# Kernel optimization log

Hardware: AMD Instinct MI355X
Metric: run time of the kernel (lower is better)

Reference implementation:

```python
import jax, jax.numpy as jnp
import numpy as np

EPS = 1e-08

def setup_inputs() -> dict:
    key = jax.random.key(0)
    k1, k2, k3 = jax.random.split(key, 3)
    R, N, E, F, O = 4, 10000, 2000, 128, 128
    X = jax.random.normal(k1, (N, F), dtype=jnp.float32)
    H = jax.random.uniform(k2, (R, N, E), dtype=jnp.float32)
    W = jax.random.normal(k3, (R, F, O), dtype=jnp.float32) * (1.0 / np.sqrt(F))
    relation_importance = jnp.ones((R,), dtype=jnp.float32)
    bias = jnp.zeros((O,), dtype=jnp.float32)
    return {"X": X, "H": H, "W": W, "relation_importance": relation_importance, "bias": bias}

def reference(X, H, W, relation_importance, bias):
    # Per-relation degree normalization applied as elementwise row/col scaling
    # (mathematically identical to diag(Dv^-1/2) @ H @ diag(De^-1/2)).
    D_v = jnp.sum(H, axis=2)                      # [R, N] node degrees
    D_e = jnp.sum(H, axis=1)                      # [R, E] hyperedge degrees
    dv_is = jnp.power(D_v + EPS, -0.5)            # [R, N]
    de_is = jnp.power(D_e + EPS, -0.5)            # [R, E]
    theta = H * dv_is[:, :, None] * de_is[:, None, :]   # [R, N, E]
    # theta @ theta.T @ X  computed right-to-left to avoid an NxN intermediate
    tX = jnp.einsum('rne,nf->ref', theta, X)      # [R, E, F]
    H_norm = jnp.einsum('rne,ref->rnf', theta, tX)  # [R, N, F]
    out = jnp.einsum('rnf,rfo->rno', H_norm, W)   # [R, N, O]
    gate = jax.nn.sigmoid(relation_importance)    # [R]
    final = jnp.sum(out * gate[:, None, None], axis=0)  # [N, O]
    return final + bias
```

## Files before the change

### kernel.cpp

```cpp
#include <hip/hip_runtime.h>
#include <hip/hip_bf16.h>

constexpr int R  = 4;
constexpr int NN = 10000;
constexpr int EE = 2000;
constexpr int FF = 128;
constexpr int OO = 128;
#define EPSV 1e-8f

typedef __attribute__((ext_vector_type(8))) short   bf16x8;
typedef __attribute__((ext_vector_type(4))) float   f32x4;

__device__ inline unsigned short f2bf(float x) {
    unsigned int u = __float_as_uint(x);
    unsigned int r = (u + 0x7fffu + ((u >> 16) & 1u)) >> 16;
    return (unsigned short)r;
}

__global__ __launch_bounds__(256) void k_deg(const float* __restrict__ H,
                                             float* __restrict__ dv_is,
                                             float* __restrict__ De) {
    const int r    = blockIdx.y;
    const int row0 = blockIdx.x * 16;
    const int t    = threadIdx.x;
    const float* Hr = H + (size_t)r * NN * EE;

    float cax[4] = {0.f, 0.f, 0.f, 0.f};
    float cay[4] = {0.f, 0.f, 0.f, 0.f};
    float rp[16];

    for (int j = 0; j < 16; ++j) {
        const float2* Hrow2 = (const float2*)(Hr + (size_t)(row0 + j) * EE);
        float s = 0.f;
#pragma unroll
        for (int i = 0; i < 4; ++i) {
            int e2 = t + 256 * i;
            if (e2 < EE / 2) {
                float2 v = Hrow2[e2];
                s += v.x + v.y;
                cax[i] += v.x;
                cay[i] += v.y;
            }
        }
        rp[j] = s;
    }

    __shared__ float lds[16][257];
#pragma unroll
    for (int j = 0; j < 16; ++j) lds[j][t] = rp[j];
    __syncthreads();
    const int jj = t >> 4, s0 = t & 15;
    float x = 0.f;
#pragma unroll
    for (int k = 0; k < 16; ++k) x += lds[jj][s0 + 16 * k];
    __syncthreads();
    lds[jj][s0] = x;
    __syncthreads();
    if (t < 16) {
        float sum = 0.f;
#pragma unroll
        for (int s = 0; s < 16; ++s) sum += lds[t][s];
        dv_is[r * NN + row0 + t] = rsqrtf(sum + EPSV);
    }

#pragma unroll
    for (int i = 0; i < 4; ++i) {
        int e2 = t + 256 * i;
        if (e2 < EE / 2) {
            atomicAdd(&De[r * EE + 2 * e2 + 0], cax[i]);
            atomicAdd(&De[r * EE + 2 * e2 + 1], cay[i]);
        }
    }
}

__global__ __launch_bounds__(256) void k_xt(const float* __restrict__ X,
                                            unsigned short* __restrict__ Xbt) {
    const int n0 = blockIdx.x * 64;
    const int f0 = blockIdx.y * 64;
    __shared__ float tile[64][65];
    const int t = threadIdx.x;
    {
        int nl = t >> 2;
        int fl = (t & 3) * 16;
        int n  = n0 + nl;
#pragma unroll
        for (int c = 0; c < 4; ++c) {
            float4 v = make_float4(0.f, 0.f, 0.f, 0.f);
            if (n < NN) v = *(const float4*)(X + (size_t)n * FF + f0 + fl + 4 * c);
            tile[nl][fl + 4 * c + 0] = v.x;
            tile[nl][fl + 4 * c + 1] = v.y;
            tile[nl][fl + 4 * c + 2] = v.z;
            tile[nl][fl + 4 * c + 3] = v.w;
        }
    }
    __syncthreads();
    {
        int fr = t >> 2;
        int nc = (t & 3) * 16;
        unsigned short u[16];
#pragma unroll
        for (int k = 0; k < 16; ++k) u[k] = f2bf(tile[nc + k][fr]);
        int f = f0 + fr;
        int nb = n0 + nc;
        unsigned short* dst = Xbt + (size_t)f * NN + nb;
        if (nb + 15 < NN) {
            uint4 p0, p1;
            p0.x = (unsigned)u[0]  | ((unsigned)u[1]  << 16);
            p0.y = (unsigned)u[2]  | ((unsigned)u[3]  << 16);
            p0.z = (unsigned)u[4]  | ((unsigned)u[5]  << 16);
            p0.w = (unsigned)u[6]  | ((unsigned)u[7]  << 16);
            p1.x = (unsigned)u[8]  | ((unsigned)u[9]  << 16);
            p1.y = (unsigned)u[10] | ((unsigned)u[11] << 16);
            p1.z = (unsigned)u[12] | ((unsigned)u[13] << 16);
            p1.w = (unsigned)u[14] | ((unsigned)u[15] << 16);
            *(uint4*)(dst)     = p0;
            *(uint4*)(dst + 8) = p1;
        } else {
#pragma unroll
            for (int k = 0; k < 16; ++k)
                if (nb + k < NN) dst[k] = u[k];
        }
    }
}

__device__ inline int lds_addr(int row, int byte_col) {
    return row * 128 + (byte_col ^ ((row & 7) << 4));
}

__global__ __launch_bounds__(256) void k_gemm1(const float* __restrict__ H,
                                               const unsigned short* __restrict__ Xbt,
                                               const float* __restrict__ dv_is,
                                               const float* __restrict__ De,
                                               float* __restrict__ T) {
    const int r  = blockIdx.y;
    const int e0 = blockIdx.x * 32;
    __shared__ unsigned short lA[32 * 64];
    __shared__ unsigned short lB[128 * 64];
    char* lAb = (char*)lA;
    char* lBb = (char*)lB;

    const int t = threadIdx.x;
    const int wave = t >> 6, lane = t & 63;
    const float* Hr  = H + (size_t)r * NN * EE;
    const float* dvr = dv_is + r * NN;

    f32x4 acc[2][2];
#pragma unroll
    for (int m = 0; m < 2; ++m)
#pragma unroll
        for (int n = 0; n < 2; ++n) acc[m][n] = (f32x4){0.f, 0.f, 0.f, 0.f};

    const int eg = (t & 7) * 4;
    const int np = t >> 3;
    const int bf = t >> 1;
    const int bh = (t & 1) * 32;

    for (int k0 = 0; k0 < NN; k0 += 64) {
        __syncthreads();
        {
            int n_ = k0 + 2 * np;
            float va[4] = {0.f, 0.f, 0.f, 0.f};
            float vb[4] = {0.f, 0.f, 0.f, 0.f};
            float d0 = 0.f, d1 = 0.f;
            const int eb = e0 + eg;
            const bool efull = (eb + 3) < EE;
            if (n_ < NN) {
                d0 = dvr[n_];
                const float* p = Hr + (size_t)n_ * EE + eb;
                if (efull) {
                    float4 v = *(const float4*)p;
                    va[0] = v.x; va[1] = v.y; va[2] = v.z; va[3] = v.w;
                } else {
#pragma unroll
                    for (int c = 0; c < 4; ++c)
                        if (eb + c < EE) va[c] = p[c];
                }
            }
            if (n_ + 1 < NN) {
                d1 = dvr[n_ + 1];
                const float* p = Hr + (size_t)(n_ + 1) * EE + eb;
                if (efull) {
                    float4 v = *(const float4*)p;
                    vb[0] = v.x; vb[1] = v.y; vb[2] = v.z; vb[3] = v.w;
                } else {
#pragma unroll
                    for (int c = 0; c < 4; ++c)
                        if (eb + c < EE) vb[c] = p[c];
                }
            }
#pragma unroll
            for (int j = 0; j < 4; ++j) {
                int row = eg + j;
                unsigned pk = (unsigned)f2bf(va[j] * d0) |
                              ((unsigned)f2bf(vb[j] * d1) << 16);
                *(unsigned*)(lAb + lds_addr(row, 4 * np)) = pk;
            }
        }
        {
#pragma unroll
            for (int j2 = 0; j2 < 4; ++j2) {
                int nb = bh + 8 * j2;
                uint4 v = *(const uint4*)(Xbt + (size_t)bf * NN + k0 + nb);
                *(uint4*)(lBb + lds_addr(bf, 2 * nb)) = v;
            }
        }
        __syncthreads();
        {
            const int kb = (lane >> 4) * 16;
#pragma unroll
            for (int kk = 0; kk < 2; ++kk) {
                bf16x8 a[2], b[2];
#pragma unroll
                for (int m = 0; m < 2; ++m) {
                    int row = (lane & 15) + 16 * m;
                    a[m] = *(const bf16x8*)(lAb + lds_addr(row, kk * 64 + kb));
                }
#pragma unroll
                for (int nf = 0; nf < 2; ++nf) {
                    int row = wave * 32 + (lane & 15) + 16 * nf;
                    b[nf] = *(const bf16x8*)(lBb + lds_addr(row, kk * 64 + kb));
                }
#pragma unroll
                for (int m = 0; m < 2; ++m)
#pragma unroll
                    for (int nf = 0; nf < 2; ++nf)
                        acc[m][nf] = __builtin_amdgcn_mfma_f32_16x16x32_bf16(
                            a[m], b[nf], acc[m][nf], 0, 0, 0);
            }
        }
    }
#pragma unroll
    for (int m = 0; m < 2; ++m) {
        int e_b = e0 + 16 * m + (lane >> 4) * 4;
#pragma unroll
        for (int j = 0; j < 4; ++j) {
            int e = e_b + j;
            if (e < EE) {
                float de2 = 1.0f / (De[r * EE + e] + EPSV);
#pragma unroll
                for (int nf = 0; nf < 2; ++nf) {
                    int f = wave * 32 + 16 * nf + (lane & 15);
                    T[((size_t)r * EE + e) * FF + f] = acc[m][nf][j] * de2;
                }
            }
        }
    }
}

__global__ __launch_bounds__(256) void k_v(const float* __restrict__ T,
                                           const float* __restrict__ W,
                                           const float* __restrict__ ri,
                                           unsigned short* __restrict__ Vt) {
    const int r  = blockIdx.y;
    const int e0 = blockIdx.x * 32;
    const float gate = 1.f / (1.f + expf(-ri[r]));
    __shared__ float lT[32][129];
    const int t = threadIdx.x;
    {
        int el = t >> 3, fl = (t & 7) * 16;
        int e = e0 + el;
#pragma unroll
        for (int c = 0; c < 4; ++c) {
            float4 v = make_float4(0.f, 0.f, 0.f, 0.f);
            if (e < EE) v = *(const float4*)(T + ((size_t)r * EE + e) * FF + fl + 4 * c);
            lT[el][fl + 4 * c + 0] = v.x;
            lT[el][fl + 4 * c + 1] = v.y;
            lT[el][fl + 4 * c + 2] = v.z;
            lT[el][fl + 4 * c + 3] = v.w;
        }
    }
    __syncthreads();
    const int o  = t & 127;
    const int eh = t >> 7;
    float acc[16];
#pragma unroll
    for (int k = 0; k < 16; ++k) acc[k] = 0.f;
    const float* Wr = W + (size_t)r * FF * OO + o;
#pragma unroll 4
    for (int f = 0; f < FF; ++f) {
        float w = Wr[(size_t)f * OO];
#pragma unroll
        for (int k = 0; k < 16; ++k) acc[k] += lT[eh * 16 + k][f] * w;
    }
    const int ebase = e0 + eh * 16;
    unsigned short* dst = Vt + ((size_t)r * OO + o) * EE + ebase;
    if (ebase + 15 < EE) {
        unsigned short u[16];
#pragma unroll
        for (int k = 0; k < 16; ++k) u[k] = f2bf(gate * acc[k]);
        uint4 p0, p1;
        p0.x = (unsigned)u[0]  | ((unsigned)u[1]  << 16);
        p0.y = (unsigned)u[2]  | ((unsigned)u[3]  << 16);
        p0.z = (unsigned)u[4]  | ((unsigned)u[5]  << 16);
        p0.w = (unsigned)u[6]  | ((unsigned)u[7]  << 16);
        p1.x = (unsigned)u[8]  | ((unsigned)u[9]  << 16);
        p1.y = (unsigned)u[10] | ((unsigned)u[11] << 16);
        p1.z = (unsigned)u[12] | ((unsigned)u[13] << 16);
        p1.w = (unsigned)u[14] | ((unsigned)u[15] << 16);
        *(uint4*)(dst)     = p0;
        *(uint4*)(dst + 8) = p1;
    } else {
#pragma unroll
        for (int k = 0; k < 16; ++k)
            if (ebase + k < EE) dst[k] = f2bf(gate * acc[k]);
    }
}

__global__ __launch_bounds__(256) void k_gemm2(const float* __restrict__ H,
                                               const unsigned short* __restrict__ Vt,
                                               const float* __restrict__ dv_is,
                                               const float* __restrict__ bias,
                                               float* __restrict__ out) {
    const int n0 = blockIdx.x * 16;
    __shared__ unsigned short lA[16 * 64];
    __shared__ unsigned short lB[128 * 64];
    char* lAb = (char*)lA;
    char* lBb = (char*)lB;

    const int t = threadIdx.x;
    const int wave = t >> 6, lane = t & 63;

    f32x4 acc[2];
    acc[0] = (f32x4){0.f, 0.f, 0.f, 0.f};
    acc[1] = (f32x4){0.f, 0.f, 0.f, 0.f};

    const int nl  = t >> 4;
    const int el4 = (t & 15) * 4;
    const int bo  = t >> 1;
    const int bh  = (t & 1) * 32;

    for (int r = 0; r < R; ++r) {
        const float* Hrow = H + ((size_t)r * NN + n0 + nl) * EE;
        const float dv = dv_is[r * NN + n0 + nl];
        const unsigned short* Vtr = Vt + (size_t)r * OO * EE;

        for (int ek = 0; ek < 2048; ek += 64) {
            __syncthreads();
            {
                int e = ek + el4;
                float va[4] = {0.f, 0.f, 0.f, 0.f};
                if (e + 3 < EE) {
                    float4 v = *(const float4*)(Hrow + e);
                    va[0] = v.x; va[1] = v.y; va[2] = v.z; va[3] = v.w;
                } else {
#pragma unroll
                    for (int c = 0; c < 4; ++c)
                        if (e + c < EE) va[c] = Hrow[e + c];
                }
                uint2 pk;
                pk.x = (unsigned)f2bf(va[0] * dv) | ((unsigned)f2bf(va[1] * dv) << 16);
                pk.y = (unsigned)f2bf(va[2] * dv) | ((unsigned)f2bf(va[3] * dv) << 16);
                *(uint2*)(lAb + lds_addr(nl, 2 * el4)) = pk;
            }
            {
#pragma unroll
                for (int j2 = 0; j2 < 4; ++j2) {
                    int ebo = bh + 8 * j2;
                    uint4 v = *(const uint4*)(Vtr + (size_t)bo * EE + ek + ebo);
                    *(uint4*)(lBb + lds_addr(bo, 2 * ebo)) = v;
                }
            }
            __syncthreads();
            {
                const int kb = (lane >> 4) * 16;
#pragma unroll
                for (int kk = 0; kk < 2; ++kk) {
                    int arow = lane & 15;
                    bf16x8 a = *(const bf16x8*)(lAb + lds_addr(arow, kk * 64 + kb));
#pragma unroll
                    for (int nf = 0; nf < 2; ++nf) {
                        int row = wave * 32 + (lane & 15) + 16 * nf;
                        bf16x8 b = *(const bf16x8*)(lBb + lds_addr(row, kk * 64 + kb));
                        acc[nf] = __builtin_amdgcn_mfma_f32_16x16x32_bf16(
                            a, b, acc[nf], 0, 0, 0);
                    }
                }
            }
        }
    }
    {
        int nrow = n0 + (lane >> 4) * 4;
#pragma unroll
        for (int nf = 0; nf < 2; ++nf) {
            int o = wave * 32 + 16 * nf + (lane & 15);
            float bv = bias[o];
#pragma unroll
            for (int j = 0; j < 4; ++j)
                out[(size_t)(nrow + j) * OO + o] = acc[nf][j] + bv;
        }
    }
}

extern "C" void kernel_launch(void* const* d_in, const int* in_sizes, int n_in,
                              void* d_out, int out_size, void* d_ws, size_t ws_size,
                              hipStream_t stream) {
    const float* X    = (const float*)d_in[0];
    const float* H    = (const float*)d_in[1];
    const float* W    = (const float*)d_in[2];
    const float* ri   = (const float*)d_in[3];
    const float* bias = (const float*)d_in[4];
    float* out = (float*)d_out;

    char* ws = (char*)d_ws;
    size_t off = 0;
    auto alloc = [&](size_t bytes) {
        size_t o = off;
        off += (bytes + 1023) & ~(size_t)1023;
        return o;
    };
    float*          dv_is = (float*)(ws + alloc((size_t)R * NN * 4));
    float*          De    = (float*)(ws + alloc((size_t)R * EE * 4));
    unsigned short* Xbt   = (unsigned short*)(ws + alloc((size_t)FF * NN * 2 + 4096));
    float*          T     = (float*)(ws + alloc((size_t)R * EE * FF * 4));
    unsigned short* Vt    = (unsigned short*)(ws + alloc((size_t)R * OO * EE * 2 + 4096));

    hipMemsetAsync(De, 0, (size_t)R * EE * 4, stream);

    hipLaunchKernelGGL(k_deg,   dim3(NN / 16, R),            dim3(256), 0, stream, H, dv_is, De);
    hipLaunchKernelGGL(k_xt,    dim3((NN + 63) / 64, FF / 64), dim3(256), 0, stream, X, Xbt);
    hipLaunchKernelGGL(k_gemm1, dim3((EE + 31) / 32, R),     dim3(256), 0, stream, H, Xbt, dv_is, De, T);
    hipLaunchKernelGGL(k_v,     dim3((EE + 31) / 32, R),     dim3(256), 0, stream, T, W, ri, Vt);
    hipLaunchKernelGGL(k_gemm2, dim3(NN / 16),               dim3(256), 0, stream, H, Vt, dv_is, bias, out);
}
```

Before: 851.3 us.

## Convert H to bf16 once in degree pass and reuse in both GEMMs

The degree kernel now also writes a bf16 copy of H, so both GEMMs read half the bytes and skip per-element scaling and conversion. The node scaling moves into the X transpose (one pre-scaled copy per relation) and the edge-degree atomics become a per-block partial buffer plus a separate reduction kernel. gemm1 uses larger edge tiles and splits K in two with a later sum, and gemm2 is parallelised over relations with larger node tiles, writing per-relation partials that a final kernel sums and adds the bias to. The cost is an extra 160 MB bf16 write plus larger workspace buffers and more launches.

```diff
diff --git a/kernel.cpp b/kernel.cpp
--- a/kernel.cpp
+++ b/kernel.cpp
@@ -6,6 +6,7 @@
 constexpr int EE = 2000;
 constexpr int FF = 128;
 constexpr int OO = 128;
+constexpr int NBLK = 625;
 #define EPSV 1e-8f
 
 typedef __attribute__((ext_vector_type(8))) short   bf16x8;
@@ -13,34 +14,46 @@
 
 __device__ inline unsigned short f2bf(float x) {
     unsigned int u = __float_as_uint(x);
-    unsigned int r = (u + 0x7fffu + ((u >> 16) & 1u)) >> 16;
-    return (unsigned short)r;
-}
-
-__global__ __launch_bounds__(256) void k_deg(const float* __restrict__ H,
-                                             float* __restrict__ dv_is,
-                                             float* __restrict__ De) {
-    const int r    = blockIdx.y;
-    const int row0 = blockIdx.x * 16;
-    const int t    = threadIdx.x;
-    const float* Hr = H + (size_t)r * NN * EE;
-
-    float cax[4] = {0.f, 0.f, 0.f, 0.f};
-    float cay[4] = {0.f, 0.f, 0.f, 0.f};
+    return (unsigned short)((u + 0x7fffu + ((u >> 16) & 1u)) >> 16);
+}
+
+__device__ inline int lds_addr(int row, int byte_col) {
+    return row * 128 + (byte_col ^ ((row & 7) << 4));
+}
+
+__global__ __launch_bounds__(256) void k_prep(const float* __restrict__ H,
+                                              unsigned short* __restrict__ Hb,
+                                              float* __restrict__ dv_is,
+                                              float* __restrict__ Dep) {
+    const int r = blockIdx.y, blk = blockIdx.x, row0 = blk * 16;
+    const int t = threadIdx.x;
+    const float* Hr = H + ((size_t)r * NN + row0) * EE;
+    unsigned short* Hbr = Hb + ((size_t)r * NN + row0) * EE;
+
+    float cp[8] = {0.f, 0.f, 0.f, 0.f, 0.f, 0.f, 0.f, 0.f};
     float rp[16];
 
     for (int j = 0; j < 16; ++j) {
-        const float2* Hrow2 = (const float2*)(Hr + (size_t)(row0 + j) * EE);
+        const float4* src = (const float4*)(Hr + (size_t)j * EE);
+        unsigned short* dstrow = Hbr + (size_t)j * EE;
         float s = 0.f;
-#pragma unroll
-        for (int i = 0; i < 4; ++i) {
-            int e2 = t + 256 * i;
-            if (e2 < EE / 2) {
-                float2 v = Hrow2[e2];
-                s += v.x + v.y;
-                cax[i] += v.x;
-                cay[i] += v.y;
-            }
+        {
+            float4 v = src[t];
+            s += v.x + v.y + v.z + v.w;
+            cp[0] += v.x; cp[1] += v.y; cp[2] += v.z; cp[3] += v.w;
+            uint2 pk;
+            pk.x = (unsigned)f2bf(v.x) | ((unsigned)f2bf(v.y) << 16);
+            pk.y = (unsigned)f2bf(v.z) | ((unsigned)f2bf(v.w) << 16);
+            *(uint2*)(dstrow + 4 * t) = pk;
+        }
+        if (t < 244) {
+            float4 v = src[t + 256];
+            s += v.x + v.y + v.z + v.w;
+            cp[4] += v.x; cp[5] += v.y; cp[6] += v.z; cp[7] += v.w;
+            uint2 pk;
+            pk.x = (unsigned)f2bf(v.x) | ((unsigned)f2bf(v.y) << 16);
+            pk.y = (unsigned)f2bf(v.z) | ((unsigned)f2bf(v.w) << 16);
+            *(uint2*)(dstrow + 4 * (t + 256)) = pk;
         }
         rp[j] = s;
     }
@@ -63,26 +76,34 @@
         dv_is[r * NN + row0 + t] = rsqrtf(sum + EPSV);
     }
 
-#pragma unroll
-    for (int i = 0; i < 4; ++i) {
-        int e2 = t + 256 * i;
-        if (e2 < EE / 2) {
-            atomicAdd(&De[r * EE + 2 * e2 + 0], cax[i]);
-            atomicAdd(&De[r * EE + 2 * e2 + 1], cay[i]);
-        }
-    }
+    float* Dp = Dep + (size_t)(r * NBLK + blk) * EE;
+    *(float4*)(Dp + 4 * t) = make_float4(cp[0], cp[1], cp[2], cp[3]);
+    if (t < 244)
+        *(float4*)(Dp + 4 * (t + 256)) = make_float4(cp[4], cp[5], cp[6], cp[7]);
+}
+
+__global__ __launch_bounds__(256) void k_dered(const float* __restrict__ Dep,
+                                               float* __restrict__ de2) {
+    const int g = blockIdx.x * 256 + threadIdx.x;
+    if (g >= R * EE) return;
+    const int r = g / EE, e = g - r * EE;
+    const float* p = Dep + (size_t)r * NBLK * EE + e;
+    float s = 0.f;
+    for (int b = 0; b < NBLK; ++b) s += p[(size_t)b * EE];
+    de2[g] = 1.0f / (s + EPSV);
 }
 
 __global__ __launch_bounds__(256) void k_xt(const float* __restrict__ X,
-                                            unsigned short* __restrict__ Xbt) {
+                                            const float* __restrict__ dv_is,
+                                            unsigned short* __restrict__ Xbtd) {
     const int n0 = blockIdx.x * 64;
     const int f0 = blockIdx.y * 64;
     __shared__ float tile[64][65];
+    __shared__ float dvt[4][64];
     const int t = threadIdx.x;
     {
-        int nl = t >> 2;
-        int fl = (t & 3) * 16;
-        int n  = n0 + nl;
+        int nl = t >> 2, fl = (t & 3) * 16;
+        int n = n0 + nl;
 #pragma unroll
         for (int c = 0; c < 4; ++c) {
             float4 v = make_float4(0.f, 0.f, 0.f, 0.f);
@@ -93,16 +114,20 @@
             tile[nl][fl + 4 * c + 3] = v.w;
         }
     }
+    {
+        int rr = t >> 6, nl = t & 63;
+        int n = n0 + nl;
+        dvt[rr][nl] = (n < NN) ? dv_is[rr * NN + n] : 0.f;
+    }
     __syncthreads();
-    {
-        int fr = t >> 2;
-        int nc = (t & 3) * 16;
+    const int fr = t >> 2, nc = (t & 3) * 16;
+    for (int r = 0; r < R; ++r) {
         unsigned short u[16];
 #pragma unroll
-        for (int k = 0; k < 16; ++k) u[k] = f2bf(tile[nc + k][fr]);
-        int f = f0 + fr;
-        int nb = n0 + nc;
-        unsigned short* dst = Xbt + (size_t)f * NN + nb;
+        for (int k = 0; k < 16; ++k)
+            u[k] = f2bf(tile[nc + k][fr] * dvt[r][nc + k]);
+        const int nb = n0 + nc;
+        unsigned short* dst = Xbtd + (size_t)(r * FF + f0 + fr) * NN + nb;
         if (nb + 15 < NN) {
             uint4 p0, p1;
             p0.x = (unsigned)u[0]  | ((unsigned)u[1]  << 16);
@@ -123,105 +148,74 @@
     }
 }
 
-__device__ inline int lds_addr(int row, int byte_col) {
-    return row * 128 + (byte_col ^ ((row & 7) << 4));
-}
-
-__global__ __launch_bounds__(256) void k_gemm1(const float* __restrict__ H,
-                                               const unsigned short* __restrict__ Xbt,
-                                               const float* __restrict__ dv_is,
-                                               const float* __restrict__ De,
-                                               float* __restrict__ T) {
+__global__ __launch_bounds__(256) void k_gemm1(const unsigned short* __restrict__ Hb,
+                                               const unsigned short* __restrict__ Xbtd,
+                                               const float* __restrict__ de2,
+                                               float* __restrict__ T2) {
+    const int e0 = blockIdx.x * 64;
     const int r  = blockIdx.y;
-    const int e0 = blockIdx.x * 32;
-    __shared__ unsigned short lA[32 * 64];
+    const int kz = blockIdx.z;
+    __shared__ unsigned short lA[64 * 64];
     __shared__ unsigned short lB[128 * 64];
     char* lAb = (char*)lA;
     char* lBb = (char*)lB;
 
-    const int t = threadIdx.x;
-    const int wave = t >> 6, lane = t & 63;
-    const float* Hr  = H + (size_t)r * NN * EE;
-    const float* dvr = dv_is + r * NN;
-
-    f32x4 acc[2][2];
-#pragma unroll
-    for (int m = 0; m < 2; ++m)
-#pragma unroll
-        for (int n = 0; n < 2; ++n) acc[m][n] = (f32x4){0.f, 0.f, 0.f, 0.f};
-
-    const int eg = (t & 7) * 4;
-    const int np = t >> 3;
-    const int bf = t >> 1;
+    const int t = threadIdx.x, wave = t >> 6, lane = t & 63;
+    const unsigned short* Hr = Hb + (size_t)r * NN * EE;
+    const unsigned short* Xr = Xbtd + (size_t)r * FF * NN;
+
+    f32x4 acc[4][2];
+#pragma unroll
+    for (int m = 0; m < 4; ++m)
+#pragma unroll
+        for (int nf = 0; nf < 2; ++nf) acc[m][nf] = (f32x4){0.f, 0.f, 0.f, 0.f};
+
+    const int q  = t & 15;
+    const int p0 = t >> 4;
+    const int bo = t >> 1;
     const int bh = (t & 1) * 32;
-
-    for (int k0 = 0; k0 < NN; k0 += 64) {
+    const bool eok = (e0 + 4 * q) < EE;
+
+    const int kbeg = kz * 5056;
+    const int kend = (kbeg + 5056 < 10048) ? (kbeg + 5056) : 10048;
+
+    for (int k0 = kbeg; k0 < kend; k0 += 64) {
         __syncthreads();
-        {
-            int n_ = k0 + 2 * np;
-            float va[4] = {0.f, 0.f, 0.f, 0.f};
-            float vb[4] = {0.f, 0.f, 0.f, 0.f};
-            float d0 = 0.f, d1 = 0.f;
-            const int eb = e0 + eg;
-            const bool efull = (eb + 3) < EE;
-            if (n_ < NN) {
-                d0 = dvr[n_];
-                const float* p = Hr + (size_t)n_ * EE + eb;
-                if (efull) {
-                    float4 v = *(const float4*)p;
-                    va[0] = v.x; va[1] = v.y; va[2] = v.z; va[3] = v.w;
-                } else {
-#pragma unroll
-                    for (int c = 0; c < 4; ++c)
-                        if (eb + c < EE) va[c] = p[c];
-                }
-            }
-            if (n_ + 1 < NN) {
-                d1 = dvr[n_ + 1];
-                const float* p = Hr + (size_t)(n_ + 1) * EE + eb;
-                if (efull) {
-                    float4 v = *(const float4*)p;
-                    vb[0] = v.x; vb[1] = v.y; vb[2] = v.z; vb[3] = v.w;
-                } else {
-#pragma unroll
-                    for (int c = 0; c < 4; ++c)
-                        if (eb + c < EE) vb[c] = p[c];
-                }
-            }
-#pragma unroll
-            for (int j = 0; j < 4; ++j) {
-                int row = eg + j;
-                unsigned pk = (unsigned)f2bf(va[j] * d0) |
-                              ((unsigned)f2bf(vb[j] * d1) << 16);
-                *(unsigned*)(lAb + lds_addr(row, 4 * np)) = pk;
-            }
-        }
-        {
-#pragma unroll
-            for (int j2 = 0; j2 < 4; ++j2) {
-                int nb = bh + 8 * j2;
-                uint4 v = *(const uint4*)(Xbt + (size_t)bf * NN + k0 + nb);
-                *(uint4*)(lBb + lds_addr(bf, 2 * nb)) = v;
-            }
+#pragma unroll
+        for (int h = 0; h < 2; ++h) {
+            const int np = p0 + 16 * h;
+            const int n_ = k0 + 2 * np;
+            uint2 ha = make_uint2(0u, 0u), hb2 = make_uint2(0u, 0u);
+            if (eok) {
+                if (n_ < NN)     ha  = *(const uint2*)(Hr + (size_t)n_ * EE + e0 + 4 * q);
+                if (n_ + 1 < NN) hb2 = *(const uint2*)(Hr + (size_t)(n_ + 1) * EE + e0 + 4 * q);
+            }
+            const unsigned a_[4] = {ha.x & 0xffffu, ha.x >> 16, ha.y & 0xffffu, ha.y >> 16};
+            const unsigned b_[4] = {hb2.x & 0xffffu, hb2.x >> 16, hb2.y & 0xffffu, hb2.y >> 16};
+#pragma unroll
+            for (int j = 0; j < 4; ++j)
+                *(unsigned*)(lAb + lds_addr(4 * q + j, 4 * np)) = a_[j] | (b_[j] << 16);
+        }
+#pragma unroll
+        for (int j2 = 0; j2 < 4; ++j2) {
+            const int nb = bh + 8 * j2;
+            uint4 v = *(const uint4*)(Xr + (size_t)bo * NN + k0 + nb);
+            *(uint4*)(lBb + lds_addr(bo, 2 * nb)) = v;
         }
         __syncthreads();
         {
             const int kb = (lane >> 4) * 16;
 #pragma unroll
             for (int kk = 0; kk < 2; ++kk) {
-                bf16x8 a[2], b[2];
-#pragma unroll
-                for (int m = 0; m < 2; ++m) {
-                    int row = (lane & 15) + 16 * m;
-                    a[m] = *(const bf16x8*)(lAb + lds_addr(row, kk * 64 + kb));
-                }
-#pragma unroll
-                for (int nf = 0; nf < 2; ++nf) {
-                    int row = wave * 32 + (lane & 15) + 16 * nf;
-                    b[nf] = *(const bf16x8*)(lBb + lds_addr(row, kk * 64 + kb));
-                }
-#pragma unroll
-                for (int m = 0; m < 2; ++m)
+                bf16x8 a[4], b[2];
+#pragma unroll
+                for (int m = 0; m < 4; ++m)
+                    a[m] = *(const bf16x8*)(lAb + lds_addr((lane & 15) + 16 * m, kk * 64 + kb));
+#pragma unroll
+                for (int nf = 0; nf < 2; ++nf)
+                    b[nf] = *(const bf16x8*)(lBb + lds_addr(wave * 32 + (lane & 15) + 16 * nf, kk * 64 + kb));
+#pragma unroll
+                for (int m = 0; m < 4; ++m)
 #pragma unroll
                     for (int nf = 0; nf < 2; ++nf)
                         acc[m][nf] = __builtin_amdgcn_mfma_f32_16x16x32_bf16(
@@ -229,25 +223,26 @@
             }
         }
     }
-#pragma unroll
-    for (int m = 0; m < 2; ++m) {
-        int e_b = e0 + 16 * m + (lane >> 4) * 4;
+    float* Tz = T2 + (size_t)kz * R * EE * FF;
+#pragma unroll
+    for (int m = 0; m < 4; ++m) {
+        const int eb = e0 + 16 * m + (lane >> 4) * 4;
 #pragma unroll
         for (int j = 0; j < 4; ++j) {
-            int e = e_b + j;
+            const int e = eb + j;
             if (e < EE) {
-                float de2 = 1.0f / (De[r * EE + e] + EPSV);
+                const float s = de2[r * EE + e];
 #pragma unroll
                 for (int nf = 0; nf < 2; ++nf) {
-                    int f = wave * 32 + 16 * nf + (lane & 15);
-                    T[((size_t)r * EE + e) * FF + f] = acc[m][nf][j] * de2;
+                    const int f = wave * 32 + 16 * nf + (lane & 15);
+                    Tz[((size_t)r * EE + e) * FF + f] = acc[m][nf][j] * s;
                 }
             }
         }
     }
 }
 
-__global__ __launch_bounds__(256) void k_v(const float* __restrict__ T,
+__global__ __launch_bounds__(256) void k_v(const float* __restrict__ T2,
                                            const float* __restrict__ W,
                                            const float* __restrict__ ri,
                                            unsigned short* __restrict__ Vt) {
@@ -256,13 +251,20 @@
     const float gate = 1.f / (1.f + expf(-ri[r]));
     __shared__ float lT[32][129];
     const int t = threadIdx.x;
+    const size_t HALF = (size_t)R * EE * FF;
     {
         int el = t >> 3, fl = (t & 7) * 16;
         int e = e0 + el;
 #pragma unroll
         for (int c = 0; c < 4; ++c) {
             float4 v = make_float4(0.f, 0.f, 0.f, 0.f);
-            if (e < EE) v = *(const float4*)(T + ((size_t)r * EE + e) * FF + fl + 4 * c);
+            if (e < EE) {
+                size_t idx = ((size_t)r * EE + e) * FF + fl + 4 * c;
+                float4 v0 = *(const float4*)(T2 + idx);
+                float4 v1 = *(const float4*)(T2 + HALF + idx);
+                v.x = v0.x + v1.x; v.y = v0.y + v1.y;
+                v.z = v0.z + v1.z; v.w = v0.w + v1.w;
+            }
             lT[el][fl + 4 * c + 0] = v.x;
             lT[el][fl + 4 * c + 1] = v.y;
             lT[el][fl + 4 * c + 2] = v.z;
@@ -306,89 +308,101 @@
     }
 }
 
-__global__ __launch_bounds__(256) void k_gemm2(const float* __restrict__ H,
+__global__ __launch_bounds__(256) void k_gemm2(const unsigned short* __restrict__ Hb,
                                                const unsigned short* __restrict__ Vt,
                                                const float* __restrict__ dv_is,
-                                               const float* __restrict__ bias,
-                                               float* __restrict__ out) {
-    const int n0 = blockIdx.x * 16;
-    __shared__ unsigned short lA[16 * 64];
+                                               float* __restrict__ outP) {
+    const int n0 = blockIdx.x * 64;
+    const int r  = blockIdx.y;
+    __shared__ unsigned short lA[64 * 64];
     __shared__ unsigned short lB[128 * 64];
     char* lAb = (char*)lA;
     char* lBb = (char*)lB;
 
-    const int t = threadIdx.x;
-    const int wave = t >> 6, lane = t & 63;
-
-    f32x4 acc[2];
-    acc[0] = (f32x4){0.f, 0.f, 0.f, 0.f};
-    acc[1] = (f32x4){0.f, 0.f, 0.f, 0.f};
-
-    const int nl  = t >> 4;
-    const int el4 = (t & 15) * 4;
-    const int bo  = t >> 1;
-    const int bh  = (t & 1) * 32;
-
+    const int t = threadIdx.x, wave = t >> 6, lane = t & 63;
+    const unsigned short* Hr = Hb + (size_t)r * NN * EE;
+    const unsigned short* Vr = Vt + (size_t)r * OO * EE;
+
+    f32x4 acc[4][2];
+#pragma unroll
+    for (int m = 0; m < 4; ++m)
+#pragma unroll
+        for (int nf = 0; nf < 2; ++nf) acc[m][nf] = (f32x4){0.f, 0.f, 0.f, 0.f};
+
+    const int nl = t >> 2;
+    const int eo = (t & 3) * 16;
+    const int bo = t >> 1;
+    const int bh = (t & 1) * 32;
+    const int nrow = n0 + nl;
+    const bool nok = nrow < NN;
+    const unsigned short* Arow = Hr + (size_t)nrow * EE;
+
+    for (int ek = 0; ek < 2048; ek += 64) {
+        __syncthreads();
+#pragma unroll
+        for (int h = 0; h < 2; ++h) {
+            const int e = ek + eo + 8 * h;
+            uint4 v = make_uint4(0u, 0u, 0u, 0u);
+            if (nok && (e + 7) < EE) v = *(const uint4*)(Arow + e);
+            *(uint4*)(lAb + lds_addr(nl, 2 * (eo + 8 * h))) = v;
+        }
+#pragma unroll
+        for (int j2 = 0; j2 < 4; ++j2) {
+            const int eb = bh + 8 * j2;
+            uint4 v = *(const uint4*)(Vr + (size_t)bo * EE + ek + eb);
+            *(uint4*)(lBb + lds_addr(bo, 2 * eb)) = v;
+        }
+        __syncthreads();
+        {
+            const int kb = (lane >> 4) * 16;
+#pragma unroll
+            for (int kk = 0; kk < 2; ++kk) {
+                bf16x8 a[4], b[2];
+#pragma unroll
+                for (int m = 0; m < 4; ++m)
+                    a[m] = *(const bf16x8*)(lAb + lds_addr((lane & 15) + 16 * m, kk * 64 + kb));
+#pragma unroll
+                for (int nf = 0; nf < 2; ++nf)
+                    b[nf] = *(const bf16x8*)(lBb + lds_addr(wave * 32 + (lane & 15) + 16 * nf, kk * 64 + kb));
+#pragma unroll
+                for (int m = 0; m < 4; ++m)
+#pragma unroll
+                    for (int nf = 0; nf < 2; ++nf)
+                        acc[m][nf] = __builtin_amdgcn_mfma_f32_16x16x32_bf16(
+                            a[m], b[nf], acc[m][nf], 0, 0, 0);
+            }
+        }
+    }
+#pragma unroll
+    for (int m = 0; m < 4; ++m) {
+        const int nb = n0 + 16 * m + (lane >> 4) * 4;
+#pragma unroll
+        for (int j = 0; j < 4; ++j) {
+            const int n = nb + j;
+            if (n < NN) {
+                const float dv = dv_is[r * NN + n];
+#pragma unroll
+                for (int nf = 0; nf < 2; ++nf) {
+                    const int o = wave * 32 + 16 * nf + (lane & 15);
+                    outP[((size_t)r * NN + n) * OO + o] = dv * acc[m][nf][j];
+                }
+            }
+        }
+    }
+}
+
+__global__ __launch_bounds__(256) void k_fin(const float* __restrict__ outP,
+                                             const float* __restrict__ bias,
+                                             float* __restrict__ out) {
+    const int g = blockIdx.x * 256 + threadIdx.x;
+    const int o4 = g & 31, n = g >> 5;
+    float4 s = ((const float4*)bias)[o4];
+#pragma unroll
     for (int r = 0; r < R; ++r) {
-        const float* Hrow = H + ((size_t)r * NN + n0 + nl) * EE;
-        const float dv = dv_is[r * NN + n0 + nl];
-        const unsigned short* Vtr = Vt + (size_t)r * OO * EE;
-
-        for (int ek = 0; ek < 2048; ek += 64) {
-            __syncthreads();
-            {
-                int e = ek + el4;
-                float va[4] = {0.f, 0.f, 0.f, 0.f};
-                if (e + 3 < EE) {
-                    float4 v = *(const float4*)(Hrow + e);
-                    va[0] = v.x; va[1] = v.y; va[2] = v.z; va[3] = v.w;
-                } else {
-#pragma unroll
-                    for (int c = 0; c < 4; ++c)
-                        if (e + c < EE) va[c] = Hrow[e + c];
-                }
-                uint2 pk;
-                pk.x = (unsigned)f2bf(va[0] * dv) | ((unsigned)f2bf(va[1] * dv) << 16);
-                pk.y = (unsigned)f2bf(va[2] * dv) | ((unsigned)f2bf(va[3] * dv) << 16);
-                *(uint2*)(lAb + lds_addr(nl, 2 * el4)) = pk;
-            }
-            {
-#pragma unroll
-                for (int j2 = 0; j2 < 4; ++j2) {
-                    int ebo = bh + 8 * j2;
-                    uint4 v = *(const uint4*)(Vtr + (size_t)bo * EE + ek + ebo);
-                    *(uint4*)(lBb + lds_addr(bo, 2 * ebo)) = v;
-                }
-            }
-            __syncthreads();
-            {
-                const int kb = (lane >> 4) * 16;
-#pragma unroll
-                for (int kk = 0; kk < 2; ++kk) {
-                    int arow = lane & 15;
-                    bf16x8 a = *(const bf16x8*)(lAb + lds_addr(arow, kk * 64 + kb));
-#pragma unroll
-                    for (int nf = 0; nf < 2; ++nf) {
-                        int row = wave * 32 + (lane & 15) + 16 * nf;
-                        bf16x8 b = *(const bf16x8*)(lBb + lds_addr(row, kk * 64 + kb));
-                        acc[nf] = __builtin_amdgcn_mfma_f32_16x16x32_bf16(
-                            a, b, acc[nf], 0, 0, 0);
-                    }
-                }
-            }
-        }
-    }
-    {
-        int nrow = n0 + (lane >> 4) * 4;
-#pragma unroll
-        for (int nf = 0; nf < 2; ++nf) {
-            int o = wave * 32 + 16 * nf + (lane & 15);
-            float bv = bias[o];
-#pragma unroll
-            for (int j = 0; j < 4; ++j)
-                out[(size_t)(nrow + j) * OO + o] = acc[nf][j] + bv;
-        }
-    }
+        float4 v = ((const float4*)outP)[((size_t)r * NN + n) * 32 + o4];
+        s.x += v.x; s.y += v.y; s.z += v.z; s.w += v.w;
+    }
+    ((float4*)out)[g] = s;
 }
 
 extern "C" void kernel_launch(void* const* d_in, const int* in_sizes, int n_in,
@@ -408,17 +422,20 @@
         off += (bytes + 1023) & ~(size_t)1023;
         return o;
     };
+    unsigned short* Hb    = (unsigned short*)(ws + alloc((size_t)R * NN * EE * 2 + 4096));
     float*          dv_is = (float*)(ws + alloc((size_t)R * NN * 4));
-    float*          De    = (float*)(ws + alloc((size_t)R * EE * 4));
-    unsigned short* Xbt   = (unsigned short*)(ws + alloc((size_t)FF * NN * 2 + 4096));
-    float*          T     = (float*)(ws + alloc((size_t)R * EE * FF * 4));
+    float*          de2   = (float*)(ws + alloc((size_t)R * EE * 4));
+    float*          Dep   = (float*)(ws + alloc((size_t)R * NBLK * EE * 4));
+    unsigned short* Xbtd  = (unsigned short*)(ws + alloc((size_t)R * FF * NN * 2 + 4096));
+    float*          T2    = (float*)(ws + alloc((size_t)2 * R * EE * FF * 4));
     unsigned short* Vt    = (unsigned short*)(ws + alloc((size_t)R * OO * EE * 2 + 4096));
-
-    hipMemsetAsync(De, 0, (size_t)R * EE * 4, stream);
-
-    hipLaunchKernelGGL(k_deg,   dim3(NN / 16, R),            dim3(256), 0, stream, H, dv_is, De);
-    hipLaunchKernelGGL(k_xt,    dim3((NN + 63) / 64, FF / 64), dim3(256), 0, stream, X, Xbt);
-    hipLaunchKernelGGL(k_gemm1, dim3((EE + 31) / 32, R),     dim3(256), 0, stream, H, Xbt, dv_is, De, T);
-    hipLaunchKernelGGL(k_v,     dim3((EE + 31) / 32, R),     dim3(256), 0, stream, T, W, ri, Vt);
-    hipLaunchKernelGGL(k_gemm2, dim3(NN / 16),               dim3(256), 0, stream, H, Vt, dv_is, bias, out);
-}
+    float*          outP  = (float*)(ws + alloc((size_t)R * NN * OO * 4));
+
+    hipLaunchKernelGGL(k_prep,  dim3(NBLK, R),     dim3(256), 0, stream, H, Hb, dv_is, Dep);
+    hipLaunchKernelGGL(k_dered, dim3(32),          dim3(256), 0, stream, Dep, de2);
+    hipLaunchKernelGGL(k_xt,    dim3(157, 2),      dim3(256), 0, stream, X, dv_is, Xbtd);
+    hipLaunchKernelGGL(k_gemm1, dim3(32, R, 2),    dim3(256), 0, stream, Hb, Xbtd, de2, T2);
+    hipLaunchKernelGGL(k_v,     dim3(63, R),       dim3(256), 0, stream, T2, W, ri, Vt);
+    hipLaunchKernelGGL(k_gemm2, dim3(157, R),      dim3(256), 0, stream, Hb, Vt, dv_is, outP);
+    hipLaunchKernelGGL(k_fin,   dim3(1250),        dim3(256), 0, stream, outP, bias, out);
+}
```

Result: faster. 732.1 us (-14.0%).
